# Performance work log

Measured on AMD Instinct MI355X. Metric: run time of the kernel, lower is better.

## Reference

```python
import jax, jax.numpy as jnp
import numpy as np

B, N, F_IN, H, OUT = 64, 1024, 195, 128, 64
K1, K2 = N // 2, N // 4  # ceil(0.5*N), ceil(0.5*K1)
EPS = 1e-5


def setup_inputs() -> dict:
    key = jax.random.key(0)
    ks = jax.random.split(key, 16)
    rn = lambda k, s: jax.random.normal(k, s, dtype=jnp.float32) * 0.1
    inp = {
        "input": jax.random.normal(ks[0], (B, N, F_IN), dtype=jnp.float32),
        # SAGEConv1 (195->128): lin_l (neighbors, w/ bias), lin_r (root, no bias)
        "W1l": rn(ks[1], (H, F_IN)), "b1l": jnp.zeros((H,), jnp.float32),
        "W1r": rn(ks[2], (H, F_IN)),
        # SAGPooling1 GNN = GraphConv(128->1): lin_rel (sum aggr, w/ bias), lin_root (no bias)
        "Wp1_rel": rn(ks[3], (1, H)), "bp1_rel": jnp.zeros((1,), jnp.float32),
        "Wp1_root": rn(ks[4], (1, H)),
        # SAGEConv2 (128->64)
        "W2l": rn(ks[5], (OUT, H)), "b2l": jnp.zeros((OUT,), jnp.float32),
        "W2r": rn(ks[6], (OUT, H)),
        # SAGPooling2 GNN = GraphConv(64->1)
        "Wp2_rel": rn(ks[7], (1, OUT)), "bp2_rel": jnp.zeros((1,), jnp.float32),
        "Wp2_root": rn(ks[8], (1, OUT)),
        # MLP head
        "fc1_w": rn(ks[9], (512, OUT)), "fc1_b": jnp.zeros((512,), jnp.float32),
        "bn1_g": jnp.ones((512,), jnp.float32), "bn1_b": jnp.zeros((512,), jnp.float32),
        "bn1_m": jnp.zeros((512,), jnp.float32), "bn1_v": jnp.ones((512,), jnp.float32),
        "fc2_w": rn(ks[10], (256, 512)), "fc2_b": jnp.zeros((256,), jnp.float32),
        "bn2_g": jnp.ones((256,), jnp.float32), "bn2_b": jnp.zeros((256,), jnp.float32),
        "bn2_m": jnp.zeros((256,), jnp.float32), "bn2_v": jnp.ones((256,), jnp.float32),
        "fc3_w": rn(ks[11], (2, 256)), "fc3_b": jnp.zeros((2,), jnp.float32),
    }
    return inp


def _corr_adj(x):
    # Pearson corrcoef over rows of x [B,N,F] -> boolean adjacency [B,N,N] (corr > 0.5)
    xc = x - x.mean(axis=-1, keepdims=True)
    cov = jnp.einsum("bnf,bmf->bnm", xc, xc)
    d = jnp.sqrt(jnp.clip(jnp.einsum("bnnf->bn", cov[..., None] * 0 + 0) + jnp.diagonal(cov, axis1=1, axis2=2), 1e-12))
    corr = cov / (d[:, :, None] * d[:, None, :])
    return (corr > 0.5).astype(x.dtype)  # symmetric, includes self-loops


def _sage(x, A, Wl, bl, Wr):
    # PyG SAGEConv: lin_l(mean_{j in N(i)} x_j) + lin_r(x_i)
    deg = A.sum(axis=-1, keepdims=True)
    agg = jnp.einsum("bnm,bmf->bnf", A, x) / jnp.maximum(deg, 1.0)
    return jnp.einsum("bnf,hf->bnh", agg, Wl) + bl + jnp.einsum("bnf,hf->bnh", x, Wr)


def _sagpool(x, A, Wrel, brel, Wroot, k):
    # score via GraphConv (sum aggr): lin_rel(sum_j x_j) + lin_root(x_i)
    agg = jnp.einsum("bnm,bmf->bnf", A, x)
    score = (jnp.einsum("bnf,of->bno", agg, Wrel) + brel
             + jnp.einsum("bnf,of->bno", x, Wroot))[..., 0]  # [B,N]
    top_s, idx = jax.lax.top_k(score, k)  # per-graph top-k nodes
    x_new = jnp.take_along_axis(x, idx[:, :, None], axis=1) * jnp.tanh(top_s)[:, :, None]
    A_new = jnp.take_along_axis(A, idx[:, :, None], axis=1)
    A_new = jnp.take_along_axis(A_new, idx[:, None, :], axis=2)
    return x_new, A_new


def _bn_eval(x, g, b, m, v):
    return g * (x - m) * jax.lax.rsqrt(v + EPS) + b


def reference(input, W1l, b1l, W1r, Wp1_rel, bp1_rel, Wp1_root,
              W2l, b2l, W2r, Wp2_rel, bp2_rel, Wp2_root,
              fc1_w, fc1_b, bn1_g, bn1_b, bn1_m, bn1_v,
              fc2_w, fc2_b, bn2_g, bn2_b, bn2_m, bn2_v,
              fc3_w, fc3_b):
    A = _corr_adj(input)                                   # [B,N,N]
    x = jax.nn.relu(_sage(input, A, W1l, b1l, W1r))        # [B,N,128]
    x, A = _sagpool(x, A, Wp1_rel, bp1_rel, Wp1_root, K1)  # [B,K1,128]
    x = jax.nn.relu(_sage(x, A, W2l, b2l, W2r))            # [B,K1,64]
    x, A = _sagpool(x, A, Wp2_rel, bp2_rel, Wp2_root, K2)  # [B,K2,64]
    x = x.mean(axis=1)                                     # global mean pool -> [B,64]
    x = _bn_eval(jax.nn.relu(x @ fc1_w.T + fc1_b), bn1_g, bn1_b, bn1_m, bn1_v)
    x = _bn_eval(jax.nn.relu(x @ fc2_w.T + fc2_b), bn2_g, bn2_b, bn2_m, bn2_v)
    x = x @ fc3_w.T + fc3_b
    return jax.nn.softmax(x, axis=1)
```

## Files before the change

### kernel.cpp

```cpp
#include <hip/hip_runtime.h>
#include <hip/hip_fp8.h>
#include <cstdint>


typedef __bf16 bf16x8 __attribute__((ext_vector_type(8)));
typedef float  floatx4 __attribute__((ext_vector_type(4)));

#define MFMA_BF16(a, b, c) __builtin_amdgcn_mfma_f32_16x16x32_bf16((a), (b), (c), 0, 0, 0)
#define MFMA_FP8(a, b, c)  __builtin_amdgcn_mfma_f32_16x16x32_fp8_fp8((a), (b), (c), 0, 0, 0)

typedef __attribute__((address_space(1))) const void as1_cvoid;
typedef __attribute__((address_space(3))) void as3_void;
static __device__ __forceinline__ void gl16(const void* g, void* l) {
  __builtin_amdgcn_global_load_lds((as1_cvoid*)g, (as3_void*)l, 16, 0, 0);
}

static constexpr int BATCH = 64, NNODE = 1024, FIN = 195, FPAD = 224;
static constexpr int HD = 128, OD = 64, KP1 = 512, KP2 = 256;

static constexpr size_t OFF_GHI   = 0;
static constexpr size_t OFF_GLO   = 8388608;
static constexpr size_t OFF_A1B   = 16777216;
static constexpr size_t OFF_YR2   = 18874368;
static constexpr size_t OFF_X2    = 35651584;
static constexpr size_t OFF_XHI   = 0;
static constexpr size_t OFF_XLO   = 29360128;
static constexpr size_t OFF_ABITS = 58720256;
static constexpr size_t OFF_X1    = 67108864;
static constexpr size_t OFF_P1    = 100663296;
static constexpr size_t OFF_Q1    = OFF_P1 + 262144;
static constexpr size_t OFF_IDX1  = OFF_Q1 + 262144;
static constexpr size_t OFF_GATE1 = OFF_IDX1 + 131072;
static constexpr size_t OFF_P2    = OFF_GATE1 + 131072;
static constexpr size_t OFF_Q2    = OFF_P2 + 131072;
static constexpr size_t OFF_W1HI  = OFF_Q2 + 131072;
static constexpr size_t OFF_W1LO  = OFF_W1HI + 114688;
static constexpr size_t OFF_W2HI  = OFF_W1LO + 114688;
static constexpr size_t OFF_W2LO  = OFF_W2HI + 32768;
static constexpr size_t OFF_FC1T  = OFF_W2LO + 32768;
static constexpr size_t OFF_FC2T  = OFF_FC1T + 131072;
static constexpr size_t OFF_XHAT  = 102760448;
static constexpr size_t OFF_YR1   = 102760448 + 16777216;

static __device__ __forceinline__ unsigned char to_fp8(float v) {
  __hip_fp8_e4m3 q(v);
  return *(unsigned char*)&q;
}

__global__ __launch_bounds__(256) void prep_pack_kernel(
    const float* __restrict__ x, __bf16* __restrict__ xhi,
    __bf16* __restrict__ xlo, unsigned char* __restrict__ xhat8,
    const float* __restrict__ W1l, const float* __restrict__ W1r,
    __bf16* __restrict__ hi1, __bf16* __restrict__ lo1,
    const float* __restrict__ W2l, const float* __restrict__ W2r,
    __bf16* __restrict__ hi2, __bf16* __restrict__ lo2,
    const float* __restrict__ fc1w, float* __restrict__ fc1t,
    const float* __restrict__ fc2w, float* __restrict__ fc2t) {
  int bid = blockIdx.x;
  if (bid < 16384) {
    int row  = bid * 4 + (threadIdx.x >> 6);
    int lane = threadIdx.x & 63;
    const float* xr = x + (long)row * FIN;
    int k0 = lane * 4;
    float v[4];
#pragma unroll
    for (int i = 0; i < 4; ++i) v[i] = (k0 + i < FIN) ? xr[k0 + i] : 0.f;
    float s = v[0] + v[1] + v[2] + v[3];
#pragma unroll
    for (int o = 32; o; o >>= 1) s += __shfl_xor(s, o);
    float mean = s * (1.f / (float)FIN);
    float c[4], ss = 0.f;
#pragma unroll
    for (int i = 0; i < 4; ++i) {
      c[i] = (k0 + i < FIN) ? (v[i] - mean) : 0.f;
      ss += c[i] * c[i];
    }
#pragma unroll
    for (int o = 32; o; o >>= 1) ss += __shfl_xor(ss, o);
    float inv = rsqrtf(fmaxf(ss, 1e-12f));
    if (k0 < FPAD) {
      __bf16 hi4[4], lo4[4];
      unsigned char h8[4];
#pragma unroll
      for (int i = 0; i < 4; ++i) {
        float xv = (k0 + i < FIN) ? v[i] : 0.f;
        __bf16 h = (__bf16)xv;
        hi4[i] = h;
        lo4[i] = (__bf16)(xv - (float)h);
        h8[i] = to_fp8(c[i] * inv);
      }
      long base = (long)row * FPAD + k0;
      *(uint2*)&xhi[base] = *(const uint2*)hi4;
      *(uint2*)&xlo[base] = *(const uint2*)lo4;
      *(unsigned int*)&xhat8[base] = *(const unsigned int*)h8;
    }
  } else if (bid < 16384 + 224) {
    int idx = (bid - 16384) * 256 + threadIdx.x;
    int h = idx / FPAD, k = idx % FPAD;
    float v = 0.f;
    if (k < FIN) v = (h < HD) ? W1l[h * FIN + k] : W1r[(h - HD) * FIN + k];
    __bf16 a = (__bf16)v;
    hi1[idx] = a;
    lo1[idx] = (__bf16)(v - (float)a);
  } else if (bid < 16672) {
    int idx = (bid - 16384 - 224) * 256 + threadIdx.x;
    int h = idx / HD, k = idx % HD;
    float v = (h < OD) ? W2l[h * HD + k] : W2r[(h - OD) * HD + k];
    __bf16 a = (__bf16)v;
    hi2[idx] = a;
    lo2[idx] = (__bf16)(v - (float)a);
  } else if (bid < 16800) {
    int idx = (bid - 16672) * 256 + threadIdx.x;
    int o = idx & 511, j = idx >> 9;
    fc1t[idx] = fc1w[o * 64 + j];
  } else {
    int idx = (bid - 16800) * 256 + threadIdx.x;
    int o = idx & 255, j = idx >> 8;
    fc2t[idx] = fc2w[o * 512 + j];
  }
}

static constexpr int CKB = 48;
__global__ __launch_bounds__(256) void corr_kernel(
    const unsigned char* __restrict__ xhat8, unsigned short* __restrict__ Abits) {
  __shared__ __align__(16) unsigned char sI[128 * CKB];
  __shared__ __align__(16) unsigned char sJ[128 * CKB];
  int bid = blockIdx.x;
  int xcd = bid & 7;
  int m = bid >> 3;
  int b = xcd + ((m & 7) << 3);
  int rem = m >> 3, bi = 0;
  while (rem >= 8 - bi) { rem -= 8 - bi; ++bi; }
  int bj = bi + rem;
  int i0 = bi * 128, j0 = bj * 128;
  const unsigned char* Xb = xhat8 + (long)b * NNODE * FPAD;
  int lane = threadIdx.x & 63, wave = threadIdx.x >> 6;
  int wi = (wave >> 1) * 64, wj = (wave & 1) * 64;
  int lr = lane & 15, lk8 = (lane >> 4) * 8;
  int strow = threadIdx.x & 127;
  int sbuf = threadIdx.x >> 7;
  floatx4 zero = {0.f, 0.f, 0.f, 0.f};
  floatx4 acc[4][4];
#pragma unroll
  for (int i = 0; i < 4; ++i)
#pragma unroll
    for (int j = 0; j < 4; ++j) acc[i][j] = zero;
  for (int kk = 0; kk < 7; ++kk) {
    int k0 = kk * 32;
    __syncthreads();
    {
      unsigned char* dst = (sbuf ? sJ : sI) + strow * CKB;
      const unsigned char* src = Xb + (long)((sbuf ? j0 : i0) + strow) * FPAD + k0;
      *(uint4*)(dst)      = *(const uint4*)(src);
      *(uint4*)(dst + 16) = *(const uint4*)(src + 16);
    }
    __syncthreads();
    long long af[4], bf[4];
#pragma unroll
    for (int t = 0; t < 4; ++t) {
      af[t] = *(const long long*)&sI[(wi + t * 16 + lr) * CKB + lk8];
      bf[t] = *(const long long*)&sJ[(wj + t * 16 + lr) * CKB + lk8];
    }
#pragma unroll
    for (int ti = 0; ti < 4; ++ti)
#pragma unroll
      for (int tj = 0; tj < 4; ++tj)
        acc[ti][tj] = MFMA_FP8(af[ti], bf[tj], acc[ti][tj]);
  }
#pragma unroll
  for (int ti = 0; ti < 4; ++ti)
#pragma unroll
    for (int tj = 0; tj < 4; ++tj) {
      floatx4 a = acc[ti][tj];
      unsigned long long m0 = __ballot(a[0] > 0.5f);
      unsigned long long m1 = __ballot(a[1] > 0.5f);
      unsigned long long m2 = __ballot(a[2] > 0.5f);
      unsigned long long m3 = __ballot(a[3] > 0.5f);
      if (lane < 16) {
        unsigned long long mm = (lane & 2) ? ((lane & 1) ? m3 : m2)
                                           : ((lane & 1) ? m1 : m0);
        unsigned short piece = (unsigned short)(mm >> ((lane >> 2) * 16));
        int grow = i0 + wi + ti * 16 + lane;
        int gcol = (j0 + wj + tj * 16) >> 4;
        Abits[((long)b * NNODE + grow) * 64 + gcol] = piece;
      }
    }
}

template <int K, int NCOL>
__global__ __launch_bounds__(256, 3) void gemm_split_kernel(
    const __bf16* __restrict__ Ahi, const __bf16* __restrict__ Alo,
    const __bf16* __restrict__ Bhi, const __bf16* __restrict__ Blo,
    float* __restrict__ C, int mblocks,
    unsigned long long* __restrict__ A64, int ntrans) {
  constexpr int ldc = NCOL * 128;
  int bid = blockIdx.x;
  if (bid >= mblocks * NCOL) {
    int t = bid - mblocks * NCOL;
    if (t >= ntrans) return;
    int b = t / 28, pi = t % 28;
    int rem = pi, rb = 1;
    while (rem >= rb) { rem -= rb; ++rb; }
    int cb = rem;
    int wave = threadIdx.x >> 6, lane = threadIdx.x & 63;
    int dr = rb * 2 + (wave >> 1);
    int dc = cb * 2 + (wave & 1);
    long base = (long)b * NNODE;
    unsigned long long xv = A64[(base + dc * 64 + lane) * 16 + dr];
    const unsigned long long M1  = 0x5555555555555555ULL;
    const unsigned long long M2  = 0x3333333333333333ULL;
    const unsigned long long M4  = 0x0F0F0F0F0F0F0F0FULL;
    const unsigned long long M8  = 0x00FF00FF00FF00FFULL;
    const unsigned long long M16 = 0x0000FFFF0000FFFFULL;
    const unsigned long long M32 = 0x00000000FFFFFFFFULL;
#define TSTEP(Kk, M)                                                      \
    {                                                                     \
      unsigned long long y = __shfl_xor(xv, Kk);                          \
      xv = ((lane & Kk) == 0) ? ((xv & (M)) | ((y & (M)) << Kk))          \
                              : ((xv & ~(M)) | ((y & ~(M)) >> Kk));       \
    }
    TSTEP(1, M1) TSTEP(2, M2) TSTEP(4, M4) TSTEP(8, M8) TSTEP(16, M16) TSTEP(32, M32)
#undef TSTEP
    A64[(base + dr * 64 + lane) * 16 + dc] = xv;
    return;
  }
  int mrow, col;
  if (NCOL == 2) {
    int xcd = bid & 7;
    int q = bid >> 3;
    col = q & 1;
    mrow = (xcd << 6) + (q >> 1);
  } else {
    mrow = bid;
    col = 0;
  }
  __shared__ __align__(16) __bf16 sAh[128 * 32];
  __shared__ __align__(16) __bf16 sAl[128 * 32];
  __shared__ __align__(16) __bf16 sBh[128 * 32];
  __shared__ __align__(16) __bf16 sBl[128 * 32];
  long row0 = (long)mrow * 128;
  int col0 = col * 128;
  int t = threadIdx.x;
  int lane = t & 63, wave = t >> 6;
  int wi = (wave >> 1) * 64, wj = (wave & 1) * 64;
  int lr = lane & 15, lk2 = (lane >> 4) * 16;
  int lk2s = lk2 ^ (((lr >> 1) & 3) << 4);
  int sr = t >> 2;
  int scb = (((t & 3) ^ ((sr >> 1) & 3)) << 4);
  const char* gA0 = (const char*)Ahi + (row0 + sr) * (long)K * 2 + scb;
  const char* gA1 = (const char*)Alo + (row0 + sr) * (long)K * 2 + scb;
  const char* gB0 = (const char*)Bhi + (long)(col0 + sr) * K * 2 + scb;
  const char* gB1 = (const char*)Blo + (long)(col0 + sr) * K * 2 + scb;
  constexpr long rstep = 64L * K * 2;
  char* lAh = (char*)sAh + (wave << 10);
  char* lAl = (char*)sAl + (wave << 10);
  char* lBh = (char*)sBh + (wave << 10);
  char* lBl = (char*)sBl + (wave << 10);
  floatx4 zero = {0.f, 0.f, 0.f, 0.f};
  floatx4 acc[4][4];
#pragma unroll
  for (int i = 0; i < 4; ++i)
#pragma unroll
    for (int j = 0; j < 4; ++j) acc[i][j] = zero;
  for (int kk = 0; kk < (K >> 5); ++kk) {
    __syncthreads();
    gl16(gA0, lAh); gl16(gA0 + rstep, lAh + 4096);
    gl16(gA1, lAl); gl16(gA1 + rstep, lAl + 4096);
    gl16(gB0, lBh); gl16(gB0 + rstep, lBh + 4096);
    gl16(gB1, lBl); gl16(gB1 + rstep, lBl + 4096);
    gA0 += 64; gA1 += 64; gB0 += 64; gB1 += 64;
    __syncthreads();
    bf16x8 bh[4], bl[4];
#pragma unroll
    for (int tj = 0; tj < 4; ++tj) {
      bh[tj] = *(const bf16x8*)((const char*)sBh + (wj + tj * 16 + lr) * 64 + lk2s);
      bl[tj] = *(const bf16x8*)((const char*)sBl + (wj + tj * 16 + lr) * 64 + lk2s);
    }
#pragma unroll
    for (int ti = 0; ti < 4; ++ti) {
      bf16x8 ah = *(const bf16x8*)((const char*)sAh + (wi + ti * 16 + lr) * 64 + lk2s);
      bf16x8 al = *(const bf16x8*)((const char*)sAl + (wi + ti * 16 + lr) * 64 + lk2s);
#pragma unroll
      for (int tj = 0; tj < 4; ++tj) acc[ti][tj] = MFMA_BF16(ah, bh[tj], acc[ti][tj]);
#pragma unroll
      for (int tj = 0; tj < 4; ++tj) acc[ti][tj] = MFMA_BF16(ah, bl[tj], acc[ti][tj]);
#pragma unroll
      for (int tj = 0; tj < 4; ++tj) acc[ti][tj] = MFMA_BF16(al, bh[tj], acc[ti][tj]);
    }
  }
#pragma unroll
  for (int ti = 0; ti < 4; ++ti)
#pragma unroll
    for (int tj = 0; tj < 4; ++tj)
#pragma unroll
      for (int rr = 0; rr < 4; ++rr) {
        long grow = row0 + wi + ti * 16 + (lane >> 4) * 4 + rr;
        int gcol = col0 + wj + tj * 16 + (lane & 15);
        C[grow * ldc + gcol] = acc[ti][tj][rr];
      }
}

__global__ __launch_bounds__(256) void sage1_kernel(
    const unsigned int* __restrict__ Abits32, const float* __restrict__ YR1,
    const float* __restrict__ b1l, const float* __restrict__ Wrel,
    const float* __restrict__ Wroot, float* __restrict__ x1,
    float* __restrict__ p1, float* __restrict__ q1) {
  int g = threadIdx.x >> 5;
  int lane = threadIdx.x & 31;
  int node = blockIdx.x * 8 + g;
  int b = node >> 10, nloc = node & 1023;
  __shared__ int list[8][1024];
  __shared__ int s_deg[8];
  {
    unsigned int word = Abits32[(long)node * 32 + lane];
    int cnt = __popc(word);
    int off = cnt;
#pragma unroll
    for (int o = 1; o < 32; o <<= 1) {
      int v = __shfl_up(off, o, 32);
      if (lane >= o) off += v;
    }
    off -= cnt;
    if (lane == 31) s_deg[g] = off + cnt;
    int basei = lane * 32;
    while (word) {
      int t = __ffs(word) - 1;
      word &= word - 1;
      list[g][off++] = basei + t;
    }
  }
  __syncthreads();
  int deg = s_deg[g];
  const float4* Y4 = (const float4*)(YR1 + (long)(b << 10) * 256);
  float4 a4 = {0.f, 0.f, 0.f, 0.f};
  for (int d = 0; d < deg; ++d) {
    float4 y = Y4[(long)list[g][d] * 64 + lane];
    a4.x += y.x; a4.y += y.y; a4.z += y.z; a4.w += y.w;
  }
  float4 R = Y4[(long)nloc * 64 + 32 + lane];
  float inv = 1.f / (float)(deg < 1 ? 1 : deg);
  float4 bl = ((const float4*)b1l)[lane];
  float4 v;
  v.x = fmaxf(a4.x * inv + bl.x + R.x, 0.f);
  v.y = fmaxf(a4.y * inv + bl.y + R.y, 0.f);
  v.z = fmaxf(a4.z * inv + bl.z + R.z, 0.f);
  v.w = fmaxf(a4.w * inv + bl.w + R.w, 0.f);
  ((float4*)x1)[(long)node * 32 + lane] = v;
  float4 wr = ((const float4*)Wrel)[lane];
  float4 wq = ((const float4*)Wroot)[lane];
  float pv = v.x * wr.x + v.y * wr.y + v.z * wr.z + v.w * wr.w;
  float qv = v.x * wq.x + v.y * wq.y + v.z * wq.z + v.w * wq.w;
#pragma unroll
  for (int o = 16; o; o >>= 1) {
    pv += __shfl_xor(pv, o, 32);
    qv += __shfl_xor(qv, o, 32);
  }
  if (lane == 0) { p1[node] = pv; q1[node] = qv; }
}

__global__ void scoretopk_kernel(const unsigned int* __restrict__ bits32,
                                 const float* __restrict__ p,
                                 const float* __restrict__ q,
                                 const float* __restrict__ brel,
                                 int* __restrict__ idx_out,
                                 float* __restrict__ gate_out,
                                 int nwords, int rpb_shift, int k) {
  int b = blockIdx.x, tid = threadIdx.x;
  int row = (b << rpb_shift) + tid;
  const unsigned int* wptr = bits32 + (long)row * nwords;
  const float* pb = p + ((long)b << rpb_shift);
  float s = q[row] + brel[0];
  for (int w = 0; w < nwords; ++w) {
    unsigned int word = wptr[w];
    while (word) {
      int t = __ffs(word) - 1;
      word &= word - 1;
      s += pb[w * 32 + t];
    }
  }
  unsigned int fb = __float_as_uint(s);
  unsigned int key = (fb & 0x80000000u) ? ~fb : (fb | 0x80000000u);
  __shared__ int hist[256];
  __shared__ unsigned int sh_prefix;
  __shared__ int sh_target, cnt_gt, cnt_eq, outpos;
  if (tid == 0) { sh_prefix = 0; sh_target = k; cnt_gt = 0; cnt_eq = 0; outpos = 0; }
  for (int shift = 24; shift >= 0; shift -= 8) {
    if (tid < 256) hist[tid] = 0;
    __syncthreads();
    unsigned int prefix = sh_prefix;
    bool inset = (shift == 24) || ((key >> (shift + 8)) == (prefix >> (shift + 8)));
    if (inset) atomicAdd(&hist[(key >> shift) & 255], 1);
    __syncthreads();
    if (tid < 64) {
      int lane = tid;
      int bb0 = hist[255 - 4 * lane];
      int bb1 = hist[254 - 4 * lane];
      int bb2 = hist[253 - 4 * lane];
      int bb3 = hist[252 - 4 * lane];
      int c0 = bb0, c1 = c0 + bb1, c2 = c1 + bb2, c3 = c2 + bb3;
      int incl = c3;
#pragma unroll
      for (int o = 1; o < 64; o <<= 1) {
        int v = __shfl_up(incl, o);
        if (lane >= o) incl += v;
      }
      int excl = incl - c3;
      int target = sh_target;
      int cum[4] = {excl + c0, excl + c1, excl + c2, excl + c3};
      int prev = excl;
#pragma unroll
      for (int i = 0; i < 4; ++i) {
        if (cum[i] >= target && prev < target) {
          int bin = 255 - (4 * lane + i);
          sh_prefix = prefix | ((unsigned int)bin << shift);
          sh_target = target - prev;
        }
        prev = cum[i];
      }
    }
    __syncthreads();
  }
  unsigned int T = sh_prefix;
  if (key > T) atomicAdd(&cnt_gt, 1);
  __syncthreads();
  int E = k - cnt_gt;
  bool sel = (key > T);
  if (!sel && key == T) sel = (atomicAdd(&cnt_eq, 1) < E);
  if (sel) {
    int posn = atomicAdd(&outpos, 1);
    idx_out[b * k + posn] = tid;
    gate_out[b * k + posn] = tanhf(s);
  }
}

__global__ __launch_bounds__(256) void gather_kernel(
    const float* __restrict__ x1, const int* __restrict__ idx,
    const float* __restrict__ gate, __bf16* __restrict__ ghi,
    __bf16* __restrict__ glo, const unsigned int* __restrict__ Abits32,
    unsigned long long* __restrict__ A1bits) {
  int bid = blockIdx.x;
  if (bid < 16384) {
    long e = (long)bid * 256 + threadIdx.x;
    int h = (int)(e & 127);
    int i = (int)((e >> 7) & 511);
    int b = (int)(e >> 16);
    int srow = idx[(b << 9) + i];
    float v = x1[((long)(b << 10) + srow) * 128 + h] * gate[(b << 9) + i];
    __bf16 a = (__bf16)v;
    ghi[e] = a;
    glo[e] = (__bf16)(v - (float)a);
  } else {
    int gi = (bid - 16384) * 4 + (threadIdx.x >> 6);
    int lane = threadIdx.x & 63;
    int b = gi >> 9;
    int srow = idx[gi];
    const unsigned int* src = Abits32 + ((long)(b << 10) + srow) * 32;
    const int* idxb = idx + (b << 9);
#pragma unroll
    for (int t = 0; t < 8; ++t) {
      int cj = idxb[t * 64 + lane];
      int bit = (src[cj >> 5] >> (cj & 31)) & 1;
      unsigned long long m = __ballot(bit);
      if (lane == 0) A1bits[(long)gi * 8 + t] = m;
    }
  }
}

__global__ __launch_bounds__(256) void sage2_kernel(
    const unsigned int* __restrict__ A1b32, const float* __restrict__ YR2,
    const float* __restrict__ b2l, const float* __restrict__ Wrel,
    const float* __restrict__ Wroot, float* __restrict__ x2,
    float* __restrict__ p2, float* __restrict__ q2) {
  int g = threadIdx.x >> 4;
  int lane = threadIdx.x & 15;
  int row = blockIdx.x * 16 + g;
  int b = row >> 9, iloc = row & 511;
  __shared__ int list[16][512];
  __shared__ int s_deg[16];
  {
    unsigned int word = A1b32[(long)row * 16 + lane];
    int cnt = __popc(word);
    int off = cnt;
#pragma unroll
    for (int o = 1; o < 16; o <<= 1) {
      int v = __shfl_up(off, o, 16);
      if (lane >= o) off += v;
    }
    off -= cnt;
    if (lane == 15) s_deg[g] = off + cnt;
    int basei = lane * 32;
    while (word) {
      int t = __ffs(word) - 1;
      word &= word - 1;
      list[g][off++] = basei + t;
    }
  }
  __syncthreads();
  int deg = s_deg[g];
  const float4* Y4 = (const float4*)(YR2 + (long)(b << 9) * 128);
  float4 a4 = {0.f, 0.f, 0.f, 0.f};
  for (int d = 0; d < deg; ++d) {
    float4 y = Y4[(long)list[g][d] * 32 + lane];
    a4.x += y.x; a4.y += y.y; a4.z += y.z; a4.w += y.w;
  }
  float4 R = Y4[(long)iloc * 32 + 16 + lane];
  float inv = 1.f / (float)(deg < 1 ? 1 : deg);
  float4 bl = ((const float4*)b2l)[lane];
  float4 v;
  v.x = fmaxf(a4.x * inv + bl.x + R.x, 0.f);
  v.y = fmaxf(a4.y * inv + bl.y + R.y, 0.f);
  v.z = fmaxf(a4.z * inv + bl.z + R.z, 0.f);
  v.w = fmaxf(a4.w * inv + bl.w + R.w, 0.f);
  ((float4*)x2)[(long)row * 16 + lane] = v;
  float4 wr = ((const float4*)Wrel)[lane];
  float4 wq = ((const float4*)Wroot)[lane];
  float pv = v.x * wr.x + v.y * wr.y + v.z * wr.z + v.w * wr.w;
  float qv = v.x * wq.x + v.y * wq.y + v.z * wq.z + v.w * wq.w;
#pragma unroll
  for (int o = 8; o; o >>= 1) {
    pv += __shfl_xor(pv, o, 16);
    qv += __shfl_xor(qv, o, 16);
  }
  if (lane == 0) { p2[row] = pv; q2[row] = qv; }
}

__global__ __launch_bounds__(512) void scoretopk_head_kernel(
    const unsigned int* __restrict__ A1b32, const float* __restrict__ p2,
    const float* __restrict__ q2, const float* __restrict__ brel,
    const float* __restrict__ x2, const float* __restrict__ fc1t,
    const float* __restrict__ fc1_b, const float* __restrict__ g1,
    const float* __restrict__ bb1, const float* __restrict__ m1,
    const float* __restrict__ v1, const float* __restrict__ fc2t,
    const float* __restrict__ fc2_b, const float* __restrict__ g2,
    const float* __restrict__ bb2, const float* __restrict__ m2,
    const float* __restrict__ v2, const float* __restrict__ fc3_w,
    const float* __restrict__ fc3_b, float* __restrict__ out) {
  int b = blockIdx.x, tid = threadIdx.x;
  int row = (b << 9) + tid;
  const unsigned int* wptr = A1b32 + (long)row * 16;
  const float* pb = p2 + ((long)b << 9);
  float s = q2[row] + brel[0];
  for (int w = 0; w < 16; ++w) {
    unsigned int word = wptr[w];
    while (word) {
      int t = __ffs(word) - 1;
      word &= word - 1;
      s += pb[w * 32 + t];
    }
  }
  constexpr int k = KP2;
  unsigned int fb = __float_as_uint(s);
  unsigned int key = (fb & 0x80000000u) ? ~fb : (fb | 0x80000000u);
  __shared__ int hist[256];
  __shared__ int idx2s[256];
  __shared__ float gate2s[256];
  __shared__ unsigned int sh_prefix;
  __shared__ int sh_target, cnt_gt, cnt_eq, outpos;
  if (tid == 0) { sh_prefix = 0; sh_target = k; cnt_gt = 0; cnt_eq = 0; outpos = 0; }
  for (int shift = 24; shift >= 0; shift -= 8) {
    if (tid < 256) hist[tid] = 0;
    __syncthreads();
    unsigned int prefix = sh_prefix;
    bool inset = (shift == 24) || ((key >> (shift + 8)) == (prefix >> (shift + 8)));
    if (inset) atomicAdd(&hist[(key >> shift) & 255], 1);
    __syncthreads();
    if (tid < 64) {
      int lane = tid;
      int bb0 = hist[255 - 4 * lane];
      int bb1 = hist[254 - 4 * lane];
      int bb2 = hist[253 - 4 * lane];
      int bb3 = hist[252 - 4 * lane];
      int c0 = bb0, c1 = c0 + bb1, c2 = c1 + bb2, c3 = c2 + bb3;
      int incl = c3;
#pragma unroll
      for (int o = 1; o < 64; o <<= 1) {
        int v = __shfl_up(incl, o);
        if (lane >= o) incl += v;
      }
      int excl = incl - c3;
      int target = sh_target;
      int cum[4] = {excl + c0, excl + c1, excl + c2, excl + c3};
      int prev = excl;
#pragma unroll
      for (int i = 0; i < 4; ++i) {
        if (cum[i] >= target && prev < target) {
          int bin = 255 - (4 * lane + i);
          sh_prefix = prefix | ((unsigned int)bin << shift);
          sh_target = target - prev;
        }
        prev = cum[i];
      }
    }
    __syncthreads();
  }
  unsigned int T = sh_prefix;
  if (key > T) atomicAdd(&cnt_gt, 1);
  __syncthreads();
  int E = k - cnt_gt;
  bool sel = (key > T);
  if (!sel && key == T) sel = (atomicAdd(&cnt_eq, 1) < E);
  if (sel) {
    int posn = atomicAdd(&outpos, 1);
    idx2s[posn] = tid;
    gate2s[posn] = tanhf(s);
  }
  __syncthreads();
  __shared__ float part[8][64];
  __shared__ float pooled[64];
  __shared__ float h1[512];
  __shared__ float h2[256];
  __shared__ float zz[2];
  int h = tid & 63, grp = tid >> 6;
  float sp = 0.f;
  for (int i = grp * 32; i < grp * 32 + 32; ++i) {
    int si = idx2s[i];
    sp += x2[((long)(b << 9) + si) * 64 + h] * gate2s[i];
  }
  part[grp][h] = sp;
  __syncthreads();
  if (tid < 64) {
    float t = 0.f;
#pragma unroll
    for (int g = 0; g < 8; ++g) t += part[g][tid];
    pooled[tid] = t * (1.f / 256.f);
  }
  __syncthreads();
  {
    float z = fc1_b[tid];
#pragma unroll 8
    for (int j = 0; j < 64; ++j) z += pooled[j] * fc1t[j * 512 + tid];
    z = fmaxf(z, 0.f);
    h1[tid] = g1[tid] * (z - m1[tid]) * rsqrtf(v1[tid] + 1e-5f) + bb1[tid];
  }
  __syncthreads();
  if (tid < 256) {
    float z = fc2_b[tid];
#pragma unroll 8
    for (int j = 0; j < 512; ++j) z += h1[j] * fc2t[j * 256 + tid];
    z = fmaxf(z, 0.f);
    h2[tid] = g2[tid] * (z - m2[tid]) * rsqrtf(v2[tid] + 1e-5f) + bb2[tid];
  }
  __syncthreads();
  if (tid < 2) {
    float z = fc3_b[tid];
    for (int j = 0; j < 256; ++j) z += h2[j] * fc3_w[tid * 256 + j];
    zz[tid] = z;
  }
  __syncthreads();
  if (tid == 0) {
    float mx = fmaxf(zz[0], zz[1]);
    float e0 = expf(zz[0] - mx), e1 = expf(zz[1] - mx);
    float inv = 1.f / (e0 + e1);
    out[b * 2 + 0] = e0 * inv;
    out[b * 2 + 1] = e1 * inv;
  }
}

extern "C" void kernel_launch(void* const* d_in, const int* in_sizes, int n_in,
                              void* d_out, int out_size, void* d_ws, size_t ws_size,
                              hipStream_t stream) {
  (void)in_sizes; (void)n_in; (void)out_size; (void)ws_size;
  const float* input   = (const float*)d_in[0];
  const float* W1l     = (const float*)d_in[1];
  const float* b1l     = (const float*)d_in[2];
  const float* W1r     = (const float*)d_in[3];
  const float* Wp1_rel = (const float*)d_in[4];
  const float* bp1_rel = (const float*)d_in[5];
  const float* Wp1_root= (const float*)d_in[6];
  const float* W2l     = (const float*)d_in[7];
  const float* b2l     = (const float*)d_in[8];
  const float* W2r     = (const float*)d_in[9];
  const float* Wp2_rel = (const float*)d_in[10];
  const float* bp2_rel = (const float*)d_in[11];
  const float* Wp2_root= (const float*)d_in[12];
  const float* fc1_w   = (const float*)d_in[13];
  const float* fc1_b   = (const float*)d_in[14];
  const float* bn1_g   = (const float*)d_in[15];
  const float* bn1_b   = (const float*)d_in[16];
  const float* bn1_m   = (const float*)d_in[17];
  const float* bn1_v   = (const float*)d_in[18];
  const float* fc2_w   = (const float*)d_in[19];
  const float* fc2_b   = (const float*)d_in[20];
  const float* bn2_g   = (const float*)d_in[21];
  const float* bn2_b   = (const float*)d_in[22];
  const float* bn2_m   = (const float*)d_in[23];
  const float* bn2_v   = (const float*)d_in[24];
  const float* fc3_w   = (const float*)d_in[25];
  const float* fc3_b   = (const float*)d_in[26];

  char* ws = (char*)d_ws;
  __bf16* xhi   = (__bf16*)(ws + OFF_XHI);
  __bf16* xlo   = (__bf16*)(ws + OFF_XLO);
  unsigned char* xhat8 = (unsigned char*)(ws + OFF_XHAT);
  unsigned short* Abits = (unsigned short*)(ws + OFF_ABITS);
  const unsigned int* Abits32 = (const unsigned int*)(ws + OFF_ABITS);
  unsigned long long* A64 = (unsigned long long*)(ws + OFF_ABITS);
  float* YR1    = (float*)(ws + OFF_YR1);
  float* x1     = (float*)(ws + OFF_X1);
  float* p1     = (float*)(ws + OFF_P1);
  float* q1     = (float*)(ws + OFF_Q1);
  int*   idx1   = (int*)(ws + OFF_IDX1);
  float* gate1  = (float*)(ws + OFF_GATE1);
  float* p2     = (float*)(ws + OFF_P2);
  float* q2     = (float*)(ws + OFF_Q2);
  __bf16* w1hi  = (__bf16*)(ws + OFF_W1HI);
  __bf16* w1lo  = (__bf16*)(ws + OFF_W1LO);
  __bf16* w2hi  = (__bf16*)(ws + OFF_W2HI);
  __bf16* w2lo  = (__bf16*)(ws + OFF_W2LO);
  float* fc1t   = (float*)(ws + OFF_FC1T);
  float* fc2t   = (float*)(ws + OFF_FC2T);
  __bf16* ghi   = (__bf16*)(ws + OFF_GHI);
  __bf16* glo   = (__bf16*)(ws + OFF_GLO);
  unsigned long long* A1bits = (unsigned long long*)(ws + OFF_A1B);
  const unsigned int* A1b32  = (const unsigned int*)(ws + OFF_A1B);
  float* YR2    = (float*)(ws + OFF_YR2);
  float* x2     = (float*)(ws + OFF_X2);
  float* out    = (float*)d_out;

  prep_pack_kernel<<<17312, 256, 0, stream>>>(input, xhi, xlo, xhat8,
                                              W1l, W1r, w1hi, w1lo,
                                              W2l, W2r, w2hi, w2lo,
                                              fc1_w, fc1t, fc2_w, fc2t);
  corr_kernel<<<2304, 256, 0, stream>>>(xhat8, Abits);
  gemm_split_kernel<224, 2><<<1024 + 1792, 256, 0, stream>>>(
      xhi, xlo, w1hi, w1lo, YR1, 512, A64, 1792);
  sage1_kernel<<<8192, 256, 0, stream>>>(Abits32, YR1, b1l, Wp1_rel, Wp1_root, x1, p1, q1);
  scoretopk_kernel<<<64, 1024, 0, stream>>>(Abits32, p1, q1, bp1_rel, idx1, gate1,
                                            32, 10, KP1);
  gather_kernel<<<24576, 256, 0, stream>>>(x1, idx1, gate1, ghi, glo, Abits32, A1bits);
  gemm_split_kernel<128, 1><<<256, 256, 0, stream>>>(
      ghi, glo, w2hi, w2lo, YR2, 256, nullptr, 0);
  sage2_kernel<<<2048, 256, 0, stream>>>(A1b32, YR2, b2l, Wp2_rel, Wp2_root, x2, p2, q2);
  scoretopk_head_kernel<<<64, 512, 0, stream>>>(A1b32, p2, q2, bp2_rel, x2,
                                                fc1t, fc1_b, bn1_g, bn1_b, bn1_m, bn1_v,
                                                fc2t, fc2_b, bn2_g, bn2_b, bn2_m, bn2_v,
                                                fc3_w, fc3_b, out);
}
```

Measured before the change: 329.5 us.

## Fuse correlation and first SAGE GEMM into one launch with in-register mirror writes

Merges the correlation-adjacency kernel and the first split-bf16 GEMM into a single launch that picks its role from the block index, sharing one LDS pool. Each off-diagonal correlation tile now also writes its transposed bit pattern directly from the ballot masks. This removes the separate shuffle-based bit-transpose blocks that the GEMM launch used to run. The intent is to save one kernel launch and one round trip over the adjacency bits, and to let the two kinds of work overlap. In exchange, register and LDS pressure is set by the larger branch, and each lane does extra scalar bit gathering plus scattered 16-bit stores.

New measurement: 322.4 us. -2.1%, faster.

```diff
diff --git a/kernel.cpp b/kernel.cpp
--- a/kernel.cpp
+++ b/kernel.cpp
@@ -121,109 +121,165 @@
 }
 
 static constexpr int CKB = 48;
-__global__ __launch_bounds__(256) void corr_kernel(
-    const unsigned char* __restrict__ xhat8, unsigned short* __restrict__ Abits) {
-  __shared__ __align__(16) unsigned char sI[128 * CKB];
-  __shared__ __align__(16) unsigned char sJ[128 * CKB];
+__global__ __launch_bounds__(256, 3) void corr_gemm1_kernel(
+    const unsigned char* __restrict__ xhat8, unsigned short* __restrict__ Abits,
+    const __bf16* __restrict__ Ahi, const __bf16* __restrict__ Alo,
+    const __bf16* __restrict__ Bhi, const __bf16* __restrict__ Blo,
+    float* __restrict__ C) {
+  __shared__ __align__(16) char pool[32768];
   int bid = blockIdx.x;
-  int xcd = bid & 7;
-  int m = bid >> 3;
-  int b = xcd + ((m & 7) << 3);
-  int rem = m >> 3, bi = 0;
-  while (rem >= 8 - bi) { rem -= 8 - bi; ++bi; }
-  int bj = bi + rem;
-  int i0 = bi * 128, j0 = bj * 128;
-  const unsigned char* Xb = xhat8 + (long)b * NNODE * FPAD;
-  int lane = threadIdx.x & 63, wave = threadIdx.x >> 6;
+  int t = threadIdx.x;
+  int lane = t & 63, wave = t >> 6;
   int wi = (wave >> 1) * 64, wj = (wave & 1) * 64;
-  int lr = lane & 15, lk8 = (lane >> 4) * 8;
-  int strow = threadIdx.x & 127;
-  int sbuf = threadIdx.x >> 7;
-  floatx4 zero = {0.f, 0.f, 0.f, 0.f};
-  floatx4 acc[4][4];
-#pragma unroll
-  for (int i = 0; i < 4; ++i)
-#pragma unroll
-    for (int j = 0; j < 4; ++j) acc[i][j] = zero;
-  for (int kk = 0; kk < 7; ++kk) {
-    int k0 = kk * 32;
-    __syncthreads();
-    {
-      unsigned char* dst = (sbuf ? sJ : sI) + strow * CKB;
-      const unsigned char* src = Xb + (long)((sbuf ? j0 : i0) + strow) * FPAD + k0;
-      *(uint4*)(dst)      = *(const uint4*)(src);
-      *(uint4*)(dst + 16) = *(const uint4*)(src + 16);
-    }
-    __syncthreads();
-    long long af[4], bf[4];
-#pragma unroll
-    for (int t = 0; t < 4; ++t) {
-      af[t] = *(const long long*)&sI[(wi + t * 16 + lr) * CKB + lk8];
-      bf[t] = *(const long long*)&sJ[(wj + t * 16 + lr) * CKB + lk8];
+  int lr = lane & 15;
+  if (bid < 2304) {
+    unsigned char* sI = (unsigned char*)pool;
+    unsigned char* sJ = (unsigned char*)pool + 128 * CKB;
+    int xcd = bid & 7;
+    int m = bid >> 3;
+    int b = xcd + ((m & 7) << 3);
+    int rem = m >> 3, bi = 0;
+    while (rem >= 8 - bi) { rem -= 8 - bi; ++bi; }
+    int bj = bi + rem;
+    int i0 = bi * 128, j0 = bj * 128;
+    const unsigned char* Xb = xhat8 + (long)b * NNODE * FPAD;
+    int lk8 = (lane >> 4) * 8;
+    int strow = t & 127;
+    int sbuf = t >> 7;
+    floatx4 zero = {0.f, 0.f, 0.f, 0.f};
+    floatx4 acc[4][4];
+#pragma unroll
+    for (int i = 0; i < 4; ++i)
+#pragma unroll
+      for (int j = 0; j < 4; ++j) acc[i][j] = zero;
+    for (int kk = 0; kk < 7; ++kk) {
+      int k0 = kk * 32;
+      __syncthreads();
+      {
+        unsigned char* dst = (sbuf ? sJ : sI) + strow * CKB;
+        const unsigned char* src = Xb + (long)((sbuf ? j0 : i0) + strow) * FPAD + k0;
+        *(uint4*)(dst)      = *(const uint4*)(src);
+        *(uint4*)(dst + 16) = *(const uint4*)(src + 16);
+      }
+      __syncthreads();
+      long long af[4], bf[4];
+#pragma unroll
+      for (int tt = 0; tt < 4; ++tt) {
+        af[tt] = *(const long long*)&sI[(wi + tt * 16 + lr) * CKB + lk8];
+        bf[tt] = *(const long long*)&sJ[(wj + tt * 16 + lr) * CKB + lk8];
+      }
+#pragma unroll
+      for (int ti = 0; ti < 4; ++ti)
+#pragma unroll
+        for (int tj = 0; tj < 4; ++tj)
+          acc[ti][tj] = MFMA_FP8(af[ti], bf[tj], acc[ti][tj]);
     }
 #pragma unroll
     for (int ti = 0; ti < 4; ++ti)
 #pragma unroll
+      for (int tj = 0; tj < 4; ++tj) {
+        floatx4 a = acc[ti][tj];
+        unsigned long long mr[4];
+        mr[0] = __ballot(a[0] > 0.5f);
+        mr[1] = __ballot(a[1] > 0.5f);
+        mr[2] = __ballot(a[2] > 0.5f);
+        mr[3] = __ballot(a[3] > 0.5f);
+        if (lane < 16) {
+          unsigned long long mm = mr[lane & 3];
+          unsigned short piece = (unsigned short)(mm >> ((lane >> 2) * 16));
+          int grow = i0 + wi + ti * 16 + lane;
+          int gcol = (j0 + wj + tj * 16) >> 4;
+          Abits[((long)b * NNODE + grow) * 64 + gcol] = piece;
+          if (bi != bj) {
+            unsigned int tp = 0;
+#pragma unroll
+            for (int tb = 0; tb < 16; ++tb)
+              tp |= (unsigned int)((mr[tb & 3] >> ((tb >> 2) * 16 + lane)) & 1ULL) << tb;
+            int grow2 = j0 + wj + tj * 16 + lane;
+            int gcol2 = (i0 + wi + ti * 16) >> 4;
+            Abits[((long)b * NNODE + grow2) * 64 + gcol2] = (unsigned short)tp;
+          }
+        }
+      }
+  } else {
+    constexpr int K = 224;
+    constexpr int ldc = 256;
+    int gid = bid - 2304;
+    int xcd = gid & 7;
+    int q = gid >> 3;
+    int col = q & 1;
+    int mrow = (xcd << 6) + (q >> 1);
+    __bf16* sAh = (__bf16*)pool;
+    __bf16* sAl = (__bf16*)(pool + 8192);
+    __bf16* sBh = (__bf16*)(pool + 16384);
+    __bf16* sBl = (__bf16*)(pool + 24576);
+    long row0 = (long)mrow * 128;
+    int col0 = col * 128;
+    int lk2 = (lane >> 4) * 16;
+    int lk2s = lk2 ^ (((lr >> 1) & 3) << 4);
+    int sr = t >> 2;
+    int scb = (((t & 3) ^ ((sr >> 1) & 3)) << 4);
+    const char* gA0 = (const char*)Ahi + (row0 + sr) * (long)K * 2 + scb;
+    const char* gA1 = (const char*)Alo + (row0 + sr) * (long)K * 2 + scb;
+    const char* gB0 = (const char*)Bhi + (long)(col0 + sr) * K * 2 + scb;
+    const char* gB1 = (const char*)Blo + (long)(col0 + sr) * K * 2 + scb;
+    constexpr long rstep = 64L * K * 2;
+    char* lAh = (char*)sAh + (wave << 10);
+    char* lAl = (char*)sAl + (wave << 10);
+    char* lBh = (char*)sBh + (wave << 10);
+    char* lBl = (char*)sBl + (wave << 10);
+    floatx4 zero = {0.f, 0.f, 0.f, 0.f};
+    floatx4 acc[4][4];
+#pragma unroll
+    for (int i = 0; i < 4; ++i)
+#pragma unroll
+      for (int j = 0; j < 4; ++j) acc[i][j] = zero;
+    for (int kk = 0; kk < (K >> 5); ++kk) {
+      __syncthreads();
+      gl16(gA0, lAh); gl16(gA0 + rstep, lAh + 4096);
+      gl16(gA1, lAl); gl16(gA1 + rstep, lAl + 4096);
+      gl16(gB0, lBh); gl16(gB0 + rstep, lBh + 4096);
+      gl16(gB1, lBl); gl16(gB1 + rstep, lBl + 4096);
+      gA0 += 64; gA1 += 64; gB0 += 64; gB1 += 64;
+      __syncthreads();
+      bf16x8 bh[4], bl[4];
+#pragma unroll
+      for (int tj = 0; tj < 4; ++tj) {
+        bh[tj] = *(const bf16x8*)((const char*)sBh + (wj + tj * 16 + lr) * 64 + lk2s);
+        bl[tj] = *(const bf16x8*)((const char*)sBl + (wj + tj * 16 + lr) * 64 + lk2s);
+      }
+#pragma unroll
+      for (int ti = 0; ti < 4; ++ti) {
+        bf16x8 ah = *(const bf16x8*)((const char*)sAh + (wi + ti * 16 + lr) * 64 + lk2s);
+        bf16x8 al = *(const bf16x8*)((const char*)sAl + (wi + ti * 16 + lr) * 64 + lk2s);
+#pragma unroll
+        for (int tj = 0; tj < 4; ++tj) acc[ti][tj] = MFMA_BF16(ah, bh[tj], acc[ti][tj]);
+#pragma unroll
+        for (int tj = 0; tj < 4; ++tj) acc[ti][tj] = MFMA_BF16(ah, bl[tj], acc[ti][tj]);
+#pragma unroll
+        for (int tj = 0; tj < 4; ++tj) acc[ti][tj] = MFMA_BF16(al, bh[tj], acc[ti][tj]);
+      }
+    }
+#pragma unroll
+    for (int ti = 0; ti < 4; ++ti)
+#pragma unroll
       for (int tj = 0; tj < 4; ++tj)
-        acc[ti][tj] = MFMA_FP8(af[ti], bf[tj], acc[ti][tj]);
-  }
-#pragma unroll
-  for (int ti = 0; ti < 4; ++ti)
-#pragma unroll
-    for (int tj = 0; tj < 4; ++tj) {
-      floatx4 a = acc[ti][tj];
-      unsigned long long m0 = __ballot(a[0] > 0.5f);
-      unsigned long long m1 = __ballot(a[1] > 0.5f);
-      unsigned long long m2 = __ballot(a[2] > 0.5f);
-      unsigned long long m3 = __ballot(a[3] > 0.5f);
-      if (lane < 16) {
-        unsigned long long mm = (lane & 2) ? ((lane & 1) ? m3 : m2)
-                                           : ((lane & 1) ? m1 : m0);
-        unsigned short piece = (unsigned short)(mm >> ((lane >> 2) * 16));
-        int grow = i0 + wi + ti * 16 + lane;
-        int gcol = (j0 + wj + tj * 16) >> 4;
-        Abits[((long)b * NNODE + grow) * 64 + gcol] = piece;
-      }
-    }
+#pragma unroll
+        for (int rr = 0; rr < 4; ++rr) {
+          long grow = row0 + wi + ti * 16 + (lane >> 4) * 4 + rr;
+          int gcol = col0 + wj + tj * 16 + (lane & 15);
+          C[grow * ldc + gcol] = acc[ti][tj][rr];
+        }
+  }
 }
 
 template <int K, int NCOL>
 __global__ __launch_bounds__(256, 3) void gemm_split_kernel(
     const __bf16* __restrict__ Ahi, const __bf16* __restrict__ Alo,
     const __bf16* __restrict__ Bhi, const __bf16* __restrict__ Blo,
-    float* __restrict__ C, int mblocks,
-    unsigned long long* __restrict__ A64, int ntrans) {
+    float* __restrict__ C) {
   constexpr int ldc = NCOL * 128;
   int bid = blockIdx.x;
-  if (bid >= mblocks * NCOL) {
-    int t = bid - mblocks * NCOL;
-    if (t >= ntrans) return;
-    int b = t / 28, pi = t % 28;
-    int rem = pi, rb = 1;
-    while (rem >= rb) { rem -= rb; ++rb; }
-    int cb = rem;
-    int wave = threadIdx.x >> 6, lane = threadIdx.x & 63;
-    int dr = rb * 2 + (wave >> 1);
-    int dc = cb * 2 + (wave & 1);
-    long base = (long)b * NNODE;
-    unsigned long long xv = A64[(base + dc * 64 + lane) * 16 + dr];
-    const unsigned long long M1  = 0x5555555555555555ULL;
-    const unsigned long long M2  = 0x3333333333333333ULL;
-    const unsigned long long M4  = 0x0F0F0F0F0F0F0F0FULL;
-    const unsigned long long M8  = 0x00FF00FF00FF00FFULL;
-    const unsigned long long M16 = 0x0000FFFF0000FFFFULL;
-    const unsigned long long M32 = 0x00000000FFFFFFFFULL;
-#define TSTEP(Kk, M)                                                      \
-    {                                                                     \
-      unsigned long long y = __shfl_xor(xv, Kk);                          \
-      xv = ((lane & Kk) == 0) ? ((xv & (M)) | ((y & (M)) << Kk))          \
-                              : ((xv & ~(M)) | ((y & ~(M)) >> Kk));       \
-    }
-    TSTEP(1, M1) TSTEP(2, M2) TSTEP(4, M4) TSTEP(8, M8) TSTEP(16, M16) TSTEP(32, M32)
-#undef TSTEP
-    A64[(base + dr * 64 + lane) * 16 + dc] = xv;
-    return;
-  }
   int mrow, col;
   if (NCOL == 2) {
     int xcd = bid & 7;
@@ -694,7 +750,6 @@
   unsigned char* xhat8 = (unsigned char*)(ws + OFF_XHAT);
   unsigned short* Abits = (unsigned short*)(ws + OFF_ABITS);
   const unsigned int* Abits32 = (const unsigned int*)(ws + OFF_ABITS);
-  unsigned long long* A64 = (unsigned long long*)(ws + OFF_ABITS);
   float* YR1    = (float*)(ws + OFF_YR1);
   float* x1     = (float*)(ws + OFF_X1);
   float* p1     = (float*)(ws + OFF_P1);
@@ -721,15 +776,14 @@
                                               W1l, W1r, w1hi, w1lo,
                                               W2l, W2r, w2hi, w2lo,
                                               fc1_w, fc1t, fc2_w, fc2t);
-  corr_kernel<<<2304, 256, 0, stream>>>(xhat8, Abits);
-  gemm_split_kernel<224, 2><<<1024 + 1792, 256, 0, stream>>>(
-      xhi, xlo, w1hi, w1lo, YR1, 512, A64, 1792);
+  corr_gemm1_kernel<<<3328, 256, 0, stream>>>(xhat8, Abits,
+                                              xhi, xlo, w1hi, w1lo, YR1);
   sage1_kernel<<<8192, 256, 0, stream>>>(Abits32, YR1, b1l, Wp1_rel, Wp1_root, x1, p1, q1);
   scoretopk_kernel<<<64, 1024, 0, stream>>>(Abits32, p1, q1, bp1_rel, idx1, gate1,
                                             32, 10, KP1);
   gather_kernel<<<24576, 256, 0, stream>>>(x1, idx1, gate1, ghi, glo, Abits32, A1bits);
   gemm_split_kernel<128, 1><<<256, 256, 0, stream>>>(
-      ghi, glo, w2hi, w2lo, YR2, 256, nullptr, 0);
+      ghi, glo, w2hi, w2lo, YR2);
   sage2_kernel<<<2048, 256, 0, stream>>>(A1b32, YR2, b2l, Wp2_rel, Wp2_root, x2, p2, q2);
   scoretopk_head_kernel<<<64, 512, 0, stream>>>(A1b32, p2, q2, bp2_rel, x2,
                                                 fc1t, fc1_b, bn1_g, bn1_b, bn1_m, bn1_v,
```
